# Kernel tuning notes

Measured on AMD Instinct MI355X. Metric: run time of the kernel, lower is better.

Reference implementation:

```python
import jax, jax.numpy as jnp
import numpy as np

B, T, D, DI, K, M, H, HD, L, VOCAB = 8, 512, 256, 512, 4, 2, 4, 64, 2, 272


def rmsnorm(x, w, eps=1e-6):
    return x * jax.lax.rsqrt(jnp.mean(x * x, axis=-1, keepdims=True) + eps) * w


def rotate_half(x):
    x1, x2 = x[..., ::2], x[..., 1::2]
    return jnp.stack([-x2, x1], axis=-1).reshape(x.shape)


def causal_conv(x, w, b):
    # x: [B,T,C], w: [C,K] depthwise causal conv, then silu
    y = jax.lax.conv_general_dilated(
        x.transpose(0, 2, 1), w[:, None, :],
        window_strides=(1,), padding=[(K - 1, 0)],
        feature_group_count=x.shape[-1])
    return jax.nn.silu(y.transpose(0, 2, 1) + b)


def delta_memory(x, Wv, Wg, Wb, Wa, A_log, dt_bias, Wblend, Wout):
    # x: [B,T,D]; per-timestep delta-rule fast-weight update with decay + key rotation
    Bv, Tn, Dm = x.shape
    vals = (x @ Wv).reshape(Bv, Tn, M, H, HD)
    gate = jax.nn.sigmoid(x @ Wg)                                   # [B,T,H]
    beta = jax.nn.sigmoid(jnp.einsum('btd,mdh->btmh', x, Wb))       # [B,T,M,H]
    alpha = jnp.einsum('btd,mdh->btmh', x, Wa) + dt_bias            # [B,T,M,H]
    decay = jnp.exp(-jnp.exp(A_log)[None, None] * jax.nn.softplus(alpha))
    blend = jax.nn.softmax((x @ Wblend).reshape(Bv, Tn, H, M), axis=-1)
    rk0 = x.reshape(Bv, Tn, H, HD)
    rk0 = rk0 / jnp.maximum(jnp.linalg.norm(rk0, axis=-1, keepdims=True), 1e-12)
    rks = [rk0]
    for _ in range(M - 1):
        rks.append(rotate_half(rks[-1]))
    rks = jnp.stack(rks, axis=2)                                    # [B,T,M,H,d]
    wks = jnp.pad(rks[:, :-1], ((0, 0), (1, 0), (0, 0), (0, 0), (0, 0)))  # shifted keys

    def step(S, inp):
        v, wk, rk, bt, dc, bl, g = inp
        S = S * dc[..., None, None]                                  # [B,M,H,d,d]
        pred = jnp.einsum('bmhdk,bmhd->bmhk', S, wk)
        err = (v - pred) * bt[..., None]
        S = S + wk[..., None] * err[..., None, :]                    # outer-product write
        read = jnp.einsum('bmhdk,bmhd->bmhk', S, rk)
        o = jnp.einsum('bhm,bmhk->bhk', bl, read) * g[..., None]
        return S, o

    tf = lambda a: jnp.moveaxis(a, 1, 0)
    xs = (tf(vals), tf(wks), tf(rks), tf(beta), tf(decay), tf(blend), tf(gate))
    S0 = jnp.zeros((Bv, M, H, HD, HD), x.dtype)
    _, o = jax.lax.scan(step, S0, xs)                                # [T,B,H,d]
    o = jnp.moveaxis(o, 0, 1).reshape(Bv, Tn, Dm)
    return x + o @ Wout


def setup_inputs():
    key = jax.random.key(0)
    ks = jax.random.split(key, 16)
    n = lambda k, shape, sc=0.02: jax.random.normal(k, shape, jnp.float32) * sc
    return {
        'ids': jax.random.randint(ks[0], (B, T), 0, VOCAB, jnp.int32),
        'emb': n(ks[1], (VOCAB, D)),
        'norm_w': jnp.ones((L, D), jnp.float32),
        'W_up': n(ks[2], (L, D, DI)),
        'W_gate': n(ks[3], (L, D, DI)),
        'W_down': n(ks[4], (L, DI, D)),
        'conv_w': n(ks[5], (L, DI, K), 0.1),
        'conv_b': jnp.zeros((L, DI), jnp.float32),
        'Wv': n(ks[6], (L, D, M * D)),
        'Wg': n(ks[7], (L, D, H)),
        'Wb': n(ks[8], (L, M, D, H)),
        'Wa': n(ks[9], (L, M, D, H)),
        'A_log': n(ks[10], (L, M, H), 0.5),
        'dt_bias': n(ks[11], (L, M, H), 0.5),
        'Wblend': n(ks[12], (L, D, H * M)),
        'Wout': n(ks[13], (L, D, D)),
        'final_norm_w': jnp.ones((D,), jnp.float32),
    }


def reference(ids, emb, norm_w, W_up, W_gate, W_down, conv_w, conv_b,
              Wv, Wg, Wb, Wa, A_log, dt_bias, Wblend, Wout, final_norm_w):
    x = emb[ids]
    for l in range(L):
        nx = rmsnorm(x, norm_w[l])
        h = causal_conv(nx @ W_up[l], conv_w[l], conv_b[l])
        out = (jax.nn.silu(nx @ W_gate[l]) * h) @ W_down[l]
        out = delta_memory(out, Wv[l], Wg[l], Wb[l], Wa[l],
                           A_log[l], dt_bias[l], Wblend[l], Wout[l])
        x = x + out
    return rmsnorm(x, final_norm_w) @ emb.T  # tied head
```

## Files before the change

### kernel.cpp

```cpp
#include <hip/hip_runtime.h>
#include <math.h>

#define BB 8
#define TT 512
#define DD 256
#define DIM 512
#define KW 4
#define MM 2
#define HH 4
#define HDIM 64
#define LL 2
#define VV 272

typedef __attribute__((ext_vector_type(8))) short bf16x8;
typedef __attribute__((ext_vector_type(4))) float f32x4;

__device__ __forceinline__ float sigf(float x){ return 1.f/(1.f+__expf(-x)); }
__device__ __forceinline__ float siluf(float x){ return x/(1.f+__expf(-x)); }

__device__ __forceinline__ unsigned short f2bf(float f){
  unsigned int u = __float_as_uint(f);
  unsigned int r = (u + 0x7FFFu + ((u >> 16) & 1u)) >> 16;
  return (unsigned short)r;
}
__device__ __forceinline__ float bf2f(unsigned short s){
  return __uint_as_float(((unsigned int)s) << 16);
}

__device__ __forceinline__ float xor1_add(float x){
  int y = __builtin_amdgcn_update_dpp(0, __float_as_int(x), 0xB1, 0xF, 0xF, true);
  return x + __int_as_float(y);
}
__device__ __forceinline__ float xor2_add(float x){
  int y = __builtin_amdgcn_update_dpp(0, __float_as_int(x), 0x4E, 0xF, 0xF, true);
  return x + __int_as_float(y);
}
__device__ __forceinline__ float ror4_add(float x){
  int y = __builtin_amdgcn_update_dpp(0, __float_as_int(x), 0x124, 0xF, 0xF, true);
  return x + __int_as_float(y);
}
__device__ __forceinline__ float ror8_add(float x){
  int y = __builtin_amdgcn_update_dpp(0, __float_as_int(x), 0x128, 0xF, 0xF, true);
  return x + __int_as_float(y);
}

__device__ __forceinline__ void gl_lds16(const void* g, void* l){
  __builtin_amdgcn_global_load_lds(
      (const __attribute__((address_space(1))) unsigned int*)g,
      (__attribute__((address_space(3))) unsigned int*)l,
      16, 0, 0);
}

#define LWB 589824
__global__ void k_cvt(const float* __restrict__ Wup, const float* __restrict__ Wgate,
                      const float* __restrict__ Wdown, const float* __restrict__ Wv,
                      const float* __restrict__ Wout, const float* __restrict__ emb,
                      const float* __restrict__ normw, const float* __restrict__ fnw,
                      unsigned short* __restrict__ wbf){
  int idx = blockIdx.x*256 + threadIdx.x;
  if (idx >= 2*LWB + VV*DD) return;
  float v;
  if (idx < 2*LWB){
    int l = (idx >= LWB) ? 1 : 0;
    int local = idx - l*LWB;
    if (local < 131072){ int n = local>>8, k = local&255;
      v = Wup[(size_t)l*131072 + k*DIM + n];
      if (l == 1) v *= normw[DD + k]; }
    else if (local < 262144){ local -= 131072; int n = local>>8, k = local&255;
      v = Wgate[(size_t)l*131072 + k*DIM + n];
      if (l == 1) v *= normw[DD + k]; }
    else if (local < 393216){ local -= 262144; int n = local>>9, k = local&511;
      v = Wdown[(size_t)l*131072 + k*DD + n]; }
    else if (local < 524288){ local -= 393216; int n = local>>8, k = local&255;
      v = Wv[(size_t)l*131072 + k*DIM + n]; }
    else { local -= 524288; int n = local>>8, k = local&255;
      v = Wout[(size_t)l*65536 + k*DD + n]; }
  } else {
    int k = (idx - 2*LWB) & 255;
    v = emb[idx - 2*LWB] * fnw[k];
  }
  wbf[idx] = f2bf(v);
}

__global__ void __launch_bounds__(256) k_embed_norm(const int* __restrict__ ids,
                                                    const float* __restrict__ emb,
                                                    const float* __restrict__ w,
                                                    float* __restrict__ x,
                                                    unsigned short* __restrict__ out){
  const int wv = threadIdx.x >> 6, l = threadIdx.x & 63;
  const int row = blockIdx.x*4 + wv;
  float4 v = *(const float4*)&emb[(size_t)ids[row]*DD + l*4];
  *(float4*)&x[(size_t)row*DD + l*4] = v;
  float ss = v.x*v.x + v.y*v.y + v.z*v.z + v.w*v.w;
  #pragma unroll
  for (int o = 32; o > 0; o >>= 1) ss += __shfl_xor(ss, o, 64);
  float sc = rsqrtf(ss*(1.f/DD) + 1e-6f);
  float4 wvv = *(const float4*)&w[l*4];
  ushort4 r;
  r.x = f2bf(v.x*sc*wvv.x); r.y = f2bf(v.y*sc*wvv.y);
  r.z = f2bf(v.z*sc*wvv.z); r.w = f2bf(v.w*sc*wvv.w);
  *(ushort4*)&out[(size_t)row*DD + l*4] = r;
}

template<int MODE>
__global__ void __launch_bounds__(256) k_gemm64(const unsigned short* __restrict__ A,
                                                const unsigned short* __restrict__ Bt,
                                                float* __restrict__ Cf,
                                                unsigned short* __restrict__ Cb,
                                                int N, int K){
  __shared__ unsigned short as[64][72];
  __shared__ unsigned short bs[64][72];
  const int tid = threadIdx.x;
  const int w = tid >> 6, l = tid & 63;
  const int m0 = blockIdx.y*64, n0 = blockIdx.x*64;
  const int ar = tid >> 2, ac = (tid & 3)*16;
  f32x4 acc[4] = {};
  for (int k0 = 0; k0 < K; k0 += 64){
    { const bf16x8* src = (const bf16x8*)&A[(size_t)(m0+ar)*K + k0 + ac];
      *(bf16x8*)&as[ar][ac]   = src[0];
      *(bf16x8*)&as[ar][ac+8] = src[1];
    }
    { int n = n0 + ar;
      bf16x8 z; z = (bf16x8)(short)0;
      bf16x8 b0 = z, b1 = z;
      if (n < N){
        const bf16x8* src = (const bf16x8*)&Bt[(size_t)n*K + k0 + ac];
        b0 = src[0]; b1 = src[1];
      }
      *(bf16x8*)&bs[ar][ac]   = b0;
      *(bf16x8*)&bs[ar][ac+8] = b1;
    }
    __syncthreads();
    const int mr = w*16 + (l & 15);
    const int kb = (l >> 4)*8;
    #pragma unroll
    for (int kc2 = 0; kc2 < 2; ++kc2){
      bf16x8 af = *(const bf16x8*)&as[mr][kc2*32 + kb];
      #pragma unroll
      for (int nt = 0; nt < 4; ++nt){
        bf16x8 bfr = *(const bf16x8*)&bs[nt*16 + (l & 15)][kc2*32 + kb];
        acc[nt] = __builtin_amdgcn_mfma_f32_16x16x32_bf16(af, bfr, acc[nt], 0, 0, 0);
      }
    }
    __syncthreads();
  }
  #pragma unroll
  for (int nt = 0; nt < 4; ++nt){
    int col = n0 + nt*16 + (l & 15);
    if (col < N){
      #pragma unroll
      for (int r = 0; r < 4; ++r){
        int row = m0 + w*16 + (l >> 4)*4 + r;
        if (MODE == 0 || MODE == 2) Cf[(size_t)row*N + col] = acc[nt][r];
        if (MODE == 1 || MODE == 2) Cb[(size_t)row*N + col] = f2bf(acc[nt][r]);
      }
    }
  }
}

__global__ void __launch_bounds__(256) k_gemmlogit(const float* __restrict__ X,
                                                   const float* __restrict__ pssq,
                                                   const unsigned short* __restrict__ Bt,
                                                   float* __restrict__ Cf,
                                                   int N, int K){
  __shared__ unsigned short as[64][72];
  __shared__ unsigned short bs[64][72];
  const int tid = threadIdx.x;
  const int w = tid >> 6, l = tid & 63;
  const int m0 = blockIdx.y*64, n0 = blockIdx.x*64;
  const int ar = tid >> 2, ac = (tid & 3)*16;
  const int arow = m0 + ar;
  const int ROWS = BB*TT;
  float ssq = pssq[arow] + pssq[ROWS + arow] + pssq[2*ROWS + arow] + pssq[3*ROWS + arow];
  const float sc = rsqrtf(ssq*(1.f/DD) + 1e-6f);
  f32x4 acc[4] = {};
  for (int k0 = 0; k0 < K; k0 += 64){
    { const float* src = &X[(size_t)arow*K + k0 + ac];
      #pragma unroll
      for (int j = 0; j < 4; ++j){
        float4 a = *(const float4*)&src[j*4];
        ushort4 u = make_ushort4(f2bf(a.x*sc), f2bf(a.y*sc), f2bf(a.z*sc), f2bf(a.w*sc));
        *(ushort4*)&as[ar][ac + j*4] = u;
      }
    }
    { int n = n0 + ar;
      bf16x8 z; z = (bf16x8)(short)0;
      bf16x8 b0 = z, b1 = z;
      if (n < N){
        const bf16x8* src = (const bf16x8*)&Bt[(size_t)n*K + k0 + ac];
        b0 = src[0]; b1 = src[1];
      }
      *(bf16x8*)&bs[ar][ac]   = b0;
      *(bf16x8*)&bs[ar][ac+8] = b1;
    }
    __syncthreads();
    const int mr = w*16 + (l & 15);
    const int kb = (l >> 4)*8;
    #pragma unroll
    for (int kc2 = 0; kc2 < 2; ++kc2){
      bf16x8 af = *(const bf16x8*)&as[mr][kc2*32 + kb];
      #pragma unroll
      for (int nt = 0; nt < 4; ++nt){
        bf16x8 bfr = *(const bf16x8*)&bs[nt*16 + (l & 15)][kc2*32 + kb];
        acc[nt] = __builtin_amdgcn_mfma_f32_16x16x32_bf16(af, bfr, acc[nt], 0, 0, 0);
      }
    }
    __syncthreads();
  }
  #pragma unroll
  for (int nt = 0; nt < 4; ++nt){
    int col = n0 + nt*16 + (l & 15);
    if (col < N){
      #pragma unroll
      for (int r = 0; r < 4; ++r){
        int row = m0 + w*16 + (l >> 4)*4 + r;
        Cf[(size_t)row*N + col] = acc[nt][r];
      }
    }
  }
}

template<int MODE>
__global__ void __launch_bounds__(256) k_gemm128(const unsigned short* __restrict__ A,
                                                 const unsigned short* __restrict__ Bt,
                                                 float* __restrict__ Cf,
                                                 unsigned short* __restrict__ Cb,
                                                 int N, int K){
  __shared__ unsigned short as[128][72];
  __shared__ unsigned short bs[64][72];
  const int tid = threadIdx.x;
  const int w = tid >> 6, l = tid & 63;
  const int m0 = blockIdx.y*128, n0 = blockIdx.x*64;
  const int ar = tid >> 1, ac = (tid & 1)*32;
  const int br = tid >> 2, bc = (tid & 3)*16;
  f32x4 acc[2][4] = {};
  for (int k0 = 0; k0 < K; k0 += 64){
    { const bf16x8* src = (const bf16x8*)&A[(size_t)(m0+ar)*K + k0 + ac];
      *(bf16x8*)&as[ar][ac]    = src[0];
      *(bf16x8*)&as[ar][ac+8]  = src[1];
      *(bf16x8*)&as[ar][ac+16] = src[2];
      *(bf16x8*)&as[ar][ac+24] = src[3];
    }
    { int n = n0 + br;
      bf16x8 z; z = (bf16x8)(short)0;
      bf16x8 b0 = z, b1 = z;
      if (n < N){
        const bf16x8* s = (const bf16x8*)&Bt[(size_t)n*K + k0 + bc];
        b0 = s[0]; b1 = s[1];
      }
      *(bf16x8*)&bs[br][bc]   = b0;
      *(bf16x8*)&bs[br][bc+8] = b1;
    }
    __syncthreads();
    const int lr = l & 15, kb = (l >> 4)*8;
    #pragma unroll
    for (int kc2 = 0; kc2 < 2; ++kc2){
      bf16x8 af0 = *(const bf16x8*)&as[w*32 + lr][kc2*32 + kb];
      bf16x8 af1 = *(const bf16x8*)&as[w*32 + 16 + lr][kc2*32 + kb];
      #pragma unroll
      for (int nt = 0; nt < 4; ++nt){
        bf16x8 bfr = *(const bf16x8*)&bs[nt*16 + lr][kc2*32 + kb];
        acc[0][nt] = __builtin_amdgcn_mfma_f32_16x16x32_bf16(af0, bfr, acc[0][nt], 0, 0, 0);
        acc[1][nt] = __builtin_amdgcn_mfma_f32_16x16x32_bf16(af1, bfr, acc[1][nt], 0, 0, 0);
      }
    }
    __syncthreads();
  }
  const int lr = l & 15;
  #pragma unroll
  for (int mt = 0; mt < 2; ++mt){
    #pragma unroll
    for (int nt = 0; nt < 4; ++nt){
      int col = n0 + nt*16 + lr;
      if (col < N){
        #pragma unroll
        for (int r = 0; r < 4; ++r){
          int row = m0 + w*32 + mt*16 + (l >> 4)*4 + r;
          if (MODE == 0 || MODE == 2) Cf[(size_t)row*N + col] = acc[mt][nt][r];
          if (MODE == 1 || MODE == 2) Cb[(size_t)row*N + col] = f2bf(acc[mt][nt][r]);
        }
      }
    }
  }
}

__global__ void __launch_bounds__(256) k_gemm_up(const unsigned short* __restrict__ A,
                                                 const unsigned short* __restrict__ But,
                                                 const unsigned short* __restrict__ Bgt,
                                                 unsigned short* __restrict__ Cu,
                                                 unsigned short* __restrict__ Cg){
  __shared__ unsigned short as[128][72];
  __shared__ unsigned short bu[64][72];
  __shared__ unsigned short bg[64][72];
  const int tid = threadIdx.x;
  const int w = tid >> 6, l = tid & 63;
  const int m0 = blockIdx.y*128, n0 = blockIdx.x*64;
  const int ar = tid >> 1, ac = (tid & 1)*32;
  const int br = tid >> 2, bc = (tid & 3)*16;
  f32x4 accu[2][4] = {}; f32x4 accg[2][4] = {};
  for (int k0 = 0; k0 < DD; k0 += 64){
    { const bf16x8* src = (const bf16x8*)&A[(size_t)(m0+ar)*DD + k0 + ac];
      *(bf16x8*)&as[ar][ac]    = src[0];
      *(bf16x8*)&as[ar][ac+8]  = src[1];
      *(bf16x8*)&as[ar][ac+16] = src[2];
      *(bf16x8*)&as[ar][ac+24] = src[3];
    }
    { const bf16x8* s0 = (const bf16x8*)&But[(size_t)(n0+br)*DD + k0 + bc];
      *(bf16x8*)&bu[br][bc]   = s0[0];
      *(bf16x8*)&bu[br][bc+8] = s0[1];
      const bf16x8* s1 = (const bf16x8*)&Bgt[(size_t)(n0+br)*DD + k0 + bc];
      *(bf16x8*)&bg[br][bc]   = s1[0];
      *(bf16x8*)&bg[br][bc+8] = s1[1];
    }
    __syncthreads();
    const int lr = l & 15, kb = (l >> 4)*8;
    #pragma unroll
    for (int kc2 = 0; kc2 < 2; ++kc2){
      bf16x8 af0 = *(const bf16x8*)&as[w*32 + lr][kc2*32 + kb];
      bf16x8 af1 = *(const bf16x8*)&as[w*32 + 16 + lr][kc2*32 + kb];
      #pragma unroll
      for (int nt = 0; nt < 4; ++nt){
        bf16x8 b0 = *(const bf16x8*)&bu[nt*16 + lr][kc2*32 + kb];
        accu[0][nt] = __builtin_amdgcn_mfma_f32_16x16x32_bf16(af0, b0, accu[0][nt], 0, 0, 0);
        accu[1][nt] = __builtin_amdgcn_mfma_f32_16x16x32_bf16(af1, b0, accu[1][nt], 0, 0, 0);
        bf16x8 b1 = *(const bf16x8*)&bg[nt*16 + lr][kc2*32 + kb];
        accg[0][nt] = __builtin_amdgcn_mfma_f32_16x16x32_bf16(af0, b1, accg[0][nt], 0, 0, 0);
        accg[1][nt] = __builtin_amdgcn_mfma_f32_16x16x32_bf16(af1, b1, accg[1][nt], 0, 0, 0);
      }
    }
    __syncthreads();
  }
  const int lr = l & 15;
  #pragma unroll
  for (int mt = 0; mt < 2; ++mt){
    #pragma unroll
    for (int nt = 0; nt < 4; ++nt){
      int col = n0 + nt*16 + lr;
      #pragma unroll
      for (int r = 0; r < 4; ++r){
        int row = m0 + w*32 + mt*16 + (l >> 4)*4 + r;
        Cu[(size_t)row*DIM + col] = f2bf(accu[mt][nt][r]);
        Cg[(size_t)row*DIM + col] = f2bf(accg[mt][nt][r]);
      }
    }
  }
}

__global__ void __launch_bounds__(256) k_gemm_up2(const float* __restrict__ X,
                                                  const float* __restrict__ pssq,
                                                  const unsigned short* __restrict__ But,
                                                  const unsigned short* __restrict__ Bgt,
                                                  unsigned short* __restrict__ Cu,
                                                  unsigned short* __restrict__ Cg){
  __shared__ unsigned short as[128][72];
  __shared__ unsigned short bu[64][72];
  __shared__ unsigned short bg[64][72];
  const int tid = threadIdx.x;
  const int w = tid >> 6, l = tid & 63;
  const int m0 = blockIdx.y*128, n0 = blockIdx.x*64;
  const int ar = tid >> 1, ac = (tid & 1)*32;
  const int br = tid >> 2, bc = (tid & 3)*16;
  const int arow = m0 + ar;
  const int ROWS = BB*TT;
  float ssq = pssq[arow] + pssq[ROWS + arow] + pssq[2*ROWS + arow] + pssq[3*ROWS + arow];
  const float sc = rsqrtf(ssq*(1.f/DD) + 1e-6f);
  f32x4 accu[2][4] = {}; f32x4 accg[2][4] = {};
  for (int k0 = 0; k0 < DD; k0 += 64){
    { const float* src = &X[(size_t)arow*DD + k0 + ac];
      #pragma unroll
      for (int j = 0; j < 8; ++j){
        float4 a = *(const float4*)&src[j*4];
        ushort4 u = make_ushort4(f2bf(a.x*sc), f2bf(a.y*sc), f2bf(a.z*sc), f2bf(a.w*sc));
        *(ushort4*)&as[ar][ac + j*4] = u;
      }
    }
    { const bf16x8* s0 = (const bf16x8*)&But[(size_t)(n0+br)*DD + k0 + bc];
      *(bf16x8*)&bu[br][bc]   = s0[0];
      *(bf16x8*)&bu[br][bc+8] = s0[1];
      const bf16x8* s1 = (const bf16x8*)&Bgt[(size_t)(n0+br)*DD + k0 + bc];
      *(bf16x8*)&bg[br][bc]   = s1[0];
      *(bf16x8*)&bg[br][bc+8] = s1[1];
    }
    __syncthreads();
    const int lr = l & 15, kb = (l >> 4)*8;
    #pragma unroll
    for (int kc2 = 0; kc2 < 2; ++kc2){
      bf16x8 af0 = *(const bf16x8*)&as[w*32 + lr][kc2*32 + kb];
      bf16x8 af1 = *(const bf16x8*)&as[w*32 + 16 + lr][kc2*32 + kb];
      #pragma unroll
      for (int nt = 0; nt < 4; ++nt){
        bf16x8 b0 = *(const bf16x8*)&bu[nt*16 + lr][kc2*32 + kb];
        accu[0][nt] = __builtin_amdgcn_mfma_f32_16x16x32_bf16(af0, b0, accu[0][nt], 0, 0, 0);
        accu[1][nt] = __builtin_amdgcn_mfma_f32_16x16x32_bf16(af1, b0, accu[1][nt], 0, 0, 0);
        bf16x8 b1 = *(const bf16x8*)&bg[nt*16 + lr][kc2*32 + kb];
        accg[0][nt] = __builtin_amdgcn_mfma_f32_16x16x32_bf16(af0, b1, accg[0][nt], 0, 0, 0);
        accg[1][nt] = __builtin_amdgcn_mfma_f32_16x16x32_bf16(af1, b1, accg[1][nt], 0, 0, 0);
      }
    }
    __syncthreads();
  }
  const int lr = l & 15;
  #pragma unroll
  for (int mt = 0; mt < 2; ++mt){
    #pragma unroll
    for (int nt = 0; nt < 4; ++nt){
      int col = n0 + nt*16 + lr;
      #pragma unroll
      for (int r = 0; r < 4; ++r){
        int row = m0 + w*32 + mt*16 + (l >> 4)*4 + r;
        Cu[(size_t)row*DIM + col] = f2bf(accu[mt][nt][r]);
        Cg[(size_t)row*DIM + col] = f2bf(accg[mt][nt][r]);
      }
    }
  }
}

__global__ void __launch_bounds__(256) k_gemm_wout(const float* __restrict__ p0,
                                                   const float* __restrict__ p1,
                                                   const unsigned short* __restrict__ Bt,
                                                   const float* __restrict__ y,
                                                   float* __restrict__ x,
                                                   float* __restrict__ rowssq){
  __shared__ unsigned short as[64][72];
  __shared__ unsigned short bs[64][72];
  const int tid = threadIdx.x;
  const int w = tid >> 6, l = tid & 63;
  const int m0 = blockIdx.y*64, n0 = blockIdx.x*64;
  const int ar = tid >> 2, ac = (tid & 3)*16;
  f32x4 acc[4] = {};
  for (int k0 = 0; k0 < DD; k0 += 64){
    #pragma unroll
    for (int j = 0; j < 4; ++j){
      size_t off = (size_t)(m0+ar)*DD + k0 + ac + j*4;
      float4 a = *(const float4*)&p0[off];
      float4 b = *(const float4*)&p1[off];
      a.x += b.x; a.y += b.y; a.z += b.z; a.w += b.w;
      ushort4 u = make_ushort4(f2bf(a.x), f2bf(a.y), f2bf(a.z), f2bf(a.w));
      *(ushort4*)&as[ar][ac + j*4] = u;
    }
    { const bf16x8* src = (const bf16x8*)&Bt[(size_t)(n0+ar)*DD + k0 + ac];
      *(bf16x8*)&bs[ar][ac]   = src[0];
      *(bf16x8*)&bs[ar][ac+8] = src[1];
    }
    __syncthreads();
    const int mr = w*16 + (l & 15);
    const int kb = (l >> 4)*8;
    #pragma unroll
    for (int kc2 = 0; kc2 < 2; ++kc2){
      bf16x8 af = *(const bf16x8*)&as[mr][kc2*32 + kb];
      #pragma unroll
      for (int nt = 0; nt < 4; ++nt){
        bf16x8 bfr = *(const bf16x8*)&bs[nt*16 + (l & 15)][kc2*32 + kb];
        acc[nt] = __builtin_amdgcn_mfma_f32_16x16x32_bf16(af, bfr, acc[nt], 0, 0, 0);
      }
    }
    __syncthreads();
  }
  const int ROWS = BB*TT;
  float ssq[4] = {0.f, 0.f, 0.f, 0.f};
  #pragma unroll
  for (int nt = 0; nt < 4; ++nt){
    int col = n0 + nt*16 + (l & 15);
    #pragma unroll
    for (int r = 0; r < 4; ++r){
      int row = m0 + w*16 + (l >> 4)*4 + r;
      size_t off = (size_t)row*DD + col;
      float nv = x[off] + y[off] + acc[nt][r];
      x[off] = nv;
      ssq[r] = fmaf(nv, nv, ssq[r]);
    }
  }
  #pragma unroll
  for (int r = 0; r < 4; ++r){
    float s = ssq[r];
    s = xor1_add(s); s = xor2_add(s); s = ror4_add(s); s = ror8_add(s);
    if ((l & 15) == 0){
      int row = m0 + w*16 + (l >> 4)*4 + r;
      rowssq[(size_t)blockIdx.x*ROWS + row] = s;
    }
  }
}

__global__ void k_conv(const unsigned short* __restrict__ u,
                       const unsigned short* __restrict__ g,
                       const float* __restrict__ cw, const float* __restrict__ cb,
                       unsigned short* __restrict__ hh){
  int i8 = blockIdx.x*256 + threadIdx.x;
  int cg = i8 & 63;
  int bt = i8 >> 6;
  int t  = bt & (TT-1);
  int c0 = cg*8;
  float acc[8];
  { float4 b0 = *(const float4*)&cb[c0];
    float4 b1 = *(const float4*)&cb[c0+4];
    acc[0]=b0.x; acc[1]=b0.y; acc[2]=b0.z; acc[3]=b0.w;
    acc[4]=b1.x; acc[5]=b1.y; acc[6]=b1.z; acc[7]=b1.w; }
  float wts[8][4];
  #pragma unroll
  for (int i = 0; i < 8; ++i) *(float4*)&wts[i][0] = *(const float4*)&cw[(c0+i)*KW];
  #pragma unroll
  for (int j = 0; j < KW; ++j){
    int dt_ = j - (KW-1);
    if (t + dt_ >= 0){
      bf16x8 uv = *(const bf16x8*)&u[(size_t)(bt + dt_)*DIM + c0];
      #pragma unroll
      for (int i = 0; i < 8; ++i)
        acc[i] = fmaf(bf2f((unsigned short)uv[i]), wts[i][j], acc[i]);
    }
  }
  bf16x8 gv = *(const bf16x8*)&g[(size_t)bt*DIM + c0];
  bf16x8 o;
  #pragma unroll
  for (int i = 0; i < 8; ++i){
    float h = siluf(acc[i]);
    o[i] = (short)f2bf(siluf(bf2f((unsigned short)gv[i])) * h);
  }
  *(bf16x8*)&hh[(size_t)bt*DIM + c0] = o;
}

__global__ void __launch_bounds__(256) k_fused(const float* __restrict__ y,
    const float* __restrict__ Wg, const float* __restrict__ Wb,
    const float* __restrict__ Wa, const float* __restrict__ Wbl,
    const float* __restrict__ A_log, const float* __restrict__ dtb,
    float* __restrict__ rkb, float* __restrict__ scal){
  __shared__ float s_y[4][260];
  __shared__ float s_p[4][32];
  const int wv = threadIdx.x >> 6, l = threadIdx.x & 63;
  const int row = blockIdx.x*4 + wv;

  float4 yv = *(const float4*)&y[(size_t)row*DD + l*4];
  *(float4*)&s_y[wv][l*4] = yv;

  float ss = yv.x*yv.x + yv.y*yv.y + yv.z*yv.z + yv.w*yv.w;
  ss = xor1_add(ss); ss = xor2_add(ss);
  ss = ror4_add(ss); ss = ror8_add(ss);
  float inv = 1.f / fmaxf(sqrtf(ss), 1e-12f);
  float4 rv; rv.x = yv.x*inv; rv.y = yv.y*inv; rv.z = yv.z*inv; rv.w = yv.w*inv;
  *(float4*)&rkb[(size_t)row*DD + l*4] = rv;

  __syncthreads();

  const int j = (l < 28) ? l : 27;
  const float* wp; int stride;
  if (j < 4){ wp = Wg + j; stride = HH; }
  else if (j < 12){ int m=(j-4)>>2, h=(j-4)&3; wp = Wb + (size_t)m*DD*HH + h; stride = HH; }
  else if (j < 20){ int m=(j-12)>>2, h=(j-12)&3; wp = Wa + (size_t)m*DD*HH + h; stride = HH; }
  else { wp = Wbl + (j-20); stride = HH*MM; }
  float a0=0.f,a1=0.f,a2=0.f,a3=0.f;
  #pragma unroll 4
  for (int k = 0; k < DD; k += 4){
    a0 = fmaf(s_y[wv][k+0], wp[(k+0)*stride], a0);
    a1 = fmaf(s_y[wv][k+1], wp[(k+1)*stride], a1);
    a2 = fmaf(s_y[wv][k+2], wp[(k+2)*stride], a2);
    a3 = fmaf(s_y[wv][k+3], wp[(k+3)*stride], a3);
  }
  if (l < 28) s_p[wv][l] = (a0+a1)+(a2+a3);

  __syncthreads();

  if (l < 8){
    int m = l >> 2, h = l & 3;
    float gs  = sigf(s_p[wv][h]);
    float btv = sigf(s_p[wv][4 + m*4 + h]);
    float sp  = s_p[wv][12 + m*4 + h] + dtb[m*HH + h];
    sp = (sp > 15.f) ? sp : log1pf(__expf(sp));
    float dc  = __expf(-__expf(A_log[m*HH + h]) * sp);
    float l0 = s_p[wv][20 + h*2], l1 = s_p[wv][20 + h*2 + 1];
    float mx = fmaxf(l0, l1);
    float e0 = __expf(l0-mx), e1 = __expf(l1-mx);
    float bl = (m ? e1 : e0) / (e0 + e1);
    float4 o; o.x = dc; o.y = btv; o.z = bl*gs; o.w = 0.f;
    *(float4*)&scal[((size_t)row*MM + m)*(HH*4) + h*4] = o;
  }
}

#define SSTEP(T_, WK, RK, PF, VB, SB) { \
  const float dc = SB.x, btv = SB.y, blg = SB.z; \
  const float v = VB; \
  { const int tn_ = ((T_)+2 < 64) ? (T_)+2 : 63; \
    PF = *(const float4*)&s_rk[p][tn_][dbase]; \
    VB = bf2f(s_v[p][tn_][vidx]); \
    SB = *(const float4*)&s_sc[p][tn_][0]; } \
  const float err = (v - dc*rrc)*btv; \
  float rr0=0.f, rr1=0.f; \
  { const float4 rp = WK; const float4 rc = RK; \
    float w0,w1,w2,w3,c0,c1,c2,c3; \
    if (ROT == 0){ w0=rp.x; w1=rp.y; w2=rp.z; w3=rp.w; c0=rc.x; c1=rc.y; c2=rc.z; c3=rc.w; } \
    else { w0=-rp.y; w1=rp.x; w2=-rp.w; w3=rp.z; c0=-rc.y; c1=rc.x; c2=-rc.w; c3=rc.z; } \
    S[0] = fmaf(S[0], dc, w0*err); rr0 = fmaf(S[0], c0, rr0); \
    S[1] = fmaf(S[1], dc, w1*err); rr1 = fmaf(S[1], c1, rr1); \
    S[2] = fmaf(S[2], dc, w2*err); rr0 = fmaf(S[2], c2, rr0); \
    S[3] = fmaf(S[3], dc, w3*err); rr1 = fmaf(S[3], c3, rr1); } \
  float rr = rr0 + rr1; \
  rr = xor1_add(rr); rr = xor2_add(rr); rr = ror4_add(rr); rr = ror8_add(rr); \
  rrc = rr; \
  if (seg == 0) part[(size_t)(rowchunk + (T_))*DD + h*HDIM + kq4*4 + klocal] = blg*rr; \
}

template<int ROT>
__device__ __forceinline__ void scan_body(int b, int h, int kq4, int l,
    const unsigned short* __restrict__ vals, const float* __restrict__ rkb,
    const float* __restrict__ scal, float* __restrict__ part,
    float (*s_rk)[64][64], unsigned short (*s_v)[64][8], float (*s_sc)[64][4])
{
  const int seg = l & 15, klocal = l >> 4;
  const int dbase = seg*4;
  const int vidx = (kq4 & 1)*4 + klocal;
  const int kq8 = kq4 >> 1;
  const int rowbase = b*TT;

  float S[4];
  #pragma unroll
  for (int j = 0; j < 4; ++j) S[j] = 0.f;
  const float4 Z = make_float4(0.f,0.f,0.f,0.f);
  float4 rb0 = Z, rb1 = Z, rb2 = Z, rb3 = Z;
  float vb0 = 0.f, vb1 = 0.f;
  float4 sb0 = Z, sb1 = Z;
  float rrc = 0.f;

  auto stage = [&](int c, int pbuf){
    const int r0 = rowbase + c*64;
    #pragma unroll
    for (int i = 0; i < 16; ++i){
      const float* g = rkb + (size_t)(r0 + i*4 + (l>>4))*DD + h*HDIM + (l&15)*4;
      gl_lds16(g, &s_rk[pbuf][i*4][0]);
    }
    { const unsigned short* g = vals + ((size_t)(r0 + l)*MM + ROT)*DD + h*HDIM + kq8*8;
      gl_lds16(g, &s_v[pbuf][0][0]); }
    { const float* g = scal + ((size_t)(r0 + l)*MM + ROT)*(HH*4) + h*4;
      gl_lds16(g, &s_sc[pbuf][0][0]); }
  };

  stage(0, 0);
  for (int c = 0; c < TT/64; ++c){
    const int p = c & 1;
    __syncthreads();
    if (c + 1 < TT/64) stage(c+1, p^1);
    rb0 = *(const float4*)&s_rk[p][0][dbase];
    rb1 = *(const float4*)&s_rk[p][1][dbase];
    vb0 = bf2f(s_v[p][0][vidx]); vb1 = bf2f(s_v[p][1][vidx]);
    sb0 = *(const float4*)&s_sc[p][0][0]; sb1 = *(const float4*)&s_sc[p][1][0];
    const int rowchunk = rowbase + c*64;
    for (int tt = 0; tt < 64; tt += 4){
      SSTEP(tt+0, rb3, rb0, rb2, vb0, sb0)
      SSTEP(tt+1, rb0, rb1, rb3, vb1, sb1)
      SSTEP(tt+2, rb1, rb2, rb0, vb0, sb0)
      SSTEP(tt+3, rb2, rb3, rb1, vb1, sb1)
    }
  }
}

__global__ void __launch_bounds__(64) k_scan(const unsigned short* __restrict__ vals,
                                             const float* __restrict__ rkb,
                                             const float* __restrict__ scal,
                                             float* __restrict__ partials){
  __shared__ float s_rk[2][64][64];
  __shared__ unsigned short s_v[2][64][8];
  __shared__ float s_sc[2][64][4];
  const int bi = blockIdx.x;
  const int kq4 = bi & 15;
  const int m  = (bi >> 4) & 1;
  const int h  = (bi >> 5) & 3;
  const int b  = bi >> 7;
  float* part = partials + (size_t)m*(BB*TT*DD);
  if (m == 0) scan_body<0>(b, h, kq4, threadIdx.x, vals, rkb, scal, part, s_rk, s_v, s_sc);
  else        scan_body<1>(b, h, kq4, threadIdx.x, vals, rkb, scal, part, s_rk, s_v, s_sc);
}

extern "C" void kernel_launch(void* const* d_in, const int* in_sizes, int n_in,
                              void* d_out, int out_size, void* d_ws, size_t ws_size,
                              hipStream_t stream){
  const int*   ids   = (const int*)d_in[0];
  const float* emb   = (const float*)d_in[1];
  const float* normw = (const float*)d_in[2];
  const float* Wup   = (const float*)d_in[3];
  const float* Wgate = (const float*)d_in[4];
  const float* Wdown = (const float*)d_in[5];
  const float* convw = (const float*)d_in[6];
  const float* convb = (const float*)d_in[7];
  const float* Wv    = (const float*)d_in[8];
  const float* Wg    = (const float*)d_in[9];
  const float* Wb    = (const float*)d_in[10];
  const float* Wa    = (const float*)d_in[11];
  const float* A_log = (const float*)d_in[12];
  const float* dtb   = (const float*)d_in[13];
  const float* Wbl   = (const float*)d_in[14];
  const float* Wout  = (const float*)d_in[15];
  const float* fnw   = (const float*)d_in[16];
  float* out = (float*)d_out;

  const int ROWS = BB*TT;
  const size_t MEG = 1u << 20;
  float* ws   = (float*)d_ws;
  float* x    = ws;
  unsigned short* nyb = (unsigned short*)(x + MEG);
  float* big1 = x + MEG + MEG/2;
  float* big2 = big1 + 2*MEG;
  float* y    = big2 + 2*MEG;
  float* rkb  = y    + MEG;
  float* scal = rkb  + MEG;
  float* rowssq = scal + (1u<<17);
  unsigned short* wbf = (unsigned short*)(rowssq + 4*ROWS);

  unsigned short* ub  = (unsigned short*)big1;
  unsigned short* gb  = (unsigned short*)(big1 + MEG);
  unsigned short* valsb = ub;

  { int total = 2*LWB + VV*DD;
    k_cvt<<<(total + 255)/256, 256, 0, stream>>>(Wup, Wgate, Wdown, Wv, Wout, emb,
                                                 normw, fnw, wbf); }

  k_embed_norm<<<ROWS/4, 256, 0, stream>>>(ids, emb, normw, x, nyb);

  for (int l = 0; l < LL; ++l){
    unsigned short* wl = wbf + (size_t)l*LWB;
    unsigned short* upT   = wl;
    unsigned short* gateT = wl + 131072;
    unsigned short* downT = wl + 262144;
    unsigned short* wvT   = wl + 393216;
    unsigned short* woutT = wl + 524288;

    if (l == 0)
      k_gemm_up<<<dim3(DIM/64, ROWS/128), 256, 0, stream>>>(nyb, upT, gateT, ub, gb);
    else
      k_gemm_up2<<<dim3(DIM/64, ROWS/128), 256, 0, stream>>>(x, rowssq, upT, gateT, ub, gb);
    k_conv<<<(ROWS*DIM/8)/256, 256, 0, stream>>>(ub, gb, convw + l*DIM*KW, convb + l*DIM, gb);
    k_gemm64<2><<<dim3(DD/64, ROWS/64), 256, 0, stream>>>(gb, downT, y, nyb, DD, DIM);
    k_gemm128<1><<<dim3(DIM/64, ROWS/128), 256, 0, stream>>>(nyb, wvT, nullptr, valsb, DIM, DD);
    k_fused<<<ROWS/4, 256, 0, stream>>>(y, Wg + l*DD*HH, Wb + (size_t)l*MM*DD*HH,
                                        Wa + (size_t)l*MM*DD*HH, Wbl + l*DD*HH*MM,
                                        A_log + l*MM*HH, dtb + l*MM*HH, rkb, scal);
    k_scan<<<BB*HH*MM*16, 64, 0, stream>>>(valsb, rkb, scal, big2);
    k_gemm_wout<<<dim3(DD/64, ROWS/64), 256, 0, stream>>>(big2, big2 + MEG, woutT, y, x, rowssq);
  }

  unsigned short* embT = wbf + 2*LWB;
  k_gemmlogit<<<dim3((VV+63)/64, ROWS/64), 256, 0, stream>>>(x, rowssq, embT, out, VV, DD);
}
```

Measured before the change: 284.9 us.

## Fuse causal depthwise conv and SiLU gating into the up/gate GEMM epilogue

Merges the separate conv kernel into the up/gate projection GEMM. The up-projection tile is staged in shared memory with a 3-row halo, and the halo rows are recomputed by scalar dot products per block. The epilogue then applies the causal conv, bias, SiLU and gate directly and writes only the final hidden activation. This removes one launch and the round trip of writing and re-reading the full up and gate tensors, at the cost of redundant halo compute, extra shared memory and one more barrier.

```diff
diff --git a/kernel.cpp b/kernel.cpp
--- a/kernel.cpp
+++ b/kernel.cpp
@@ -284,26 +284,89 @@
   }
 }
 
-__global__ void __launch_bounds__(256) k_gemm_up(const unsigned short* __restrict__ A,
-                                                 const unsigned short* __restrict__ But,
-                                                 const unsigned short* __restrict__ Bgt,
-                                                 unsigned short* __restrict__ Cu,
-                                                 unsigned short* __restrict__ Cg){
+template<int L>
+__global__ void __launch_bounds__(256) k_gemm_upc(
+    const unsigned short* __restrict__ Anyb,
+    const float* __restrict__ X, const float* __restrict__ pssq,
+    const unsigned short* __restrict__ But,
+    const unsigned short* __restrict__ Bgt,
+    const float* __restrict__ cw, const float* __restrict__ cb,
+    unsigned short* __restrict__ Chh)
+{
   __shared__ unsigned short as[128][72];
   __shared__ unsigned short bu[64][72];
   __shared__ unsigned short bg[64][72];
+  __shared__ unsigned short s_ub[132][68];
+  __shared__ float s_cw[64][4];
+  __shared__ float s_cb[64];
   const int tid = threadIdx.x;
   const int w = tid >> 6, l = tid & 63;
   const int m0 = blockIdx.y*128, n0 = blockIdx.x*64;
   const int ar = tid >> 1, ac = (tid & 1)*32;
   const int br = tid >> 2, bc = (tid & 3)*16;
+  const int ROWS = BB*TT;
+  const int t0 = m0 & (TT-1);
+
+  float scA = 1.f;
+  if (L == 1){
+    const int arow = m0 + ar;
+    float ssq = pssq[arow] + pssq[ROWS + arow] + pssq[2*ROWS + arow] + pssq[3*ROWS + arow];
+    scA = rsqrtf(ssq*(1.f/DD) + 1e-6f);
+  }
+
+  if (tid < 192){
+    int i = tid >> 6;
+    int c = tid & 63;
+    float acc = 0.f;
+    if (t0 != 0){
+      int grow = m0 - 3 + i;
+      const unsigned short* bptr = &But[(size_t)(n0+c)*DD];
+      if (L == 0){
+        const unsigned short* a = &Anyb[(size_t)grow*DD];
+        for (int k = 0; k < DD; k += 8){
+          bf16x8 av = *(const bf16x8*)&a[k];
+          bf16x8 bv = *(const bf16x8*)&bptr[k];
+          #pragma unroll
+          for (int e = 0; e < 8; ++e)
+            acc = fmaf(bf2f((unsigned short)av[e]), bf2f((unsigned short)bv[e]), acc);
+        }
+      } else {
+        float ssq = pssq[grow] + pssq[ROWS + grow] + pssq[2*ROWS + grow] + pssq[3*ROWS + grow];
+        float sc = rsqrtf(ssq*(1.f/DD) + 1e-6f);
+        const float* a = &X[(size_t)grow*DD];
+        for (int k = 0; k < DD; k += 4){
+          float4 av = *(const float4*)&a[k];
+          #pragma unroll
+          for (int e = 0; e < 4; ++e){
+            float ae = bf2f(f2bf(((const float*)&av)[e]*sc));
+            acc = fmaf(ae, bf2f(bptr[k+e]), acc);
+          }
+        }
+      }
+    }
+    s_ub[tid >> 6][tid & 63] = (t0 != 0) ? f2bf(acc) : (unsigned short)0;
+  }
+  if (tid < 64){
+    *(float4*)&s_cw[tid][0] = *(const float4*)&cw[(n0+tid)*KW];
+    s_cb[tid] = cb[n0+tid];
+  }
+
   f32x4 accu[2][4] = {}; f32x4 accg[2][4] = {};
   for (int k0 = 0; k0 < DD; k0 += 64){
-    { const bf16x8* src = (const bf16x8*)&A[(size_t)(m0+ar)*DD + k0 + ac];
+    if (L == 0){
+      const bf16x8* src = (const bf16x8*)&Anyb[(size_t)(m0+ar)*DD + k0 + ac];
       *(bf16x8*)&as[ar][ac]    = src[0];
       *(bf16x8*)&as[ar][ac+8]  = src[1];
       *(bf16x8*)&as[ar][ac+16] = src[2];
       *(bf16x8*)&as[ar][ac+24] = src[3];
+    } else {
+      const float* src = &X[(size_t)(m0+ar)*DD + k0 + ac];
+      #pragma unroll
+      for (int j = 0; j < 8; ++j){
+        float4 a = *(const float4*)&src[j*4];
+        ushort4 u = make_ushort4(f2bf(a.x*scA), f2bf(a.y*scA), f2bf(a.z*scA), f2bf(a.w*scA));
+        *(ushort4*)&as[ar][ac + j*4] = u;
+      }
     }
     { const bf16x8* s0 = (const bf16x8*)&But[(size_t)(n0+br)*DD + k0 + bc];
       *(bf16x8*)&bu[br][bc]   = s0[0];
@@ -330,89 +393,35 @@
     }
     __syncthreads();
   }
+
   const int lr = l & 15;
   #pragma unroll
-  for (int mt = 0; mt < 2; ++mt){
-    #pragma unroll
-    for (int nt = 0; nt < 4; ++nt){
-      int col = n0 + nt*16 + lr;
+  for (int mt = 0; mt < 2; ++mt)
+    #pragma unroll
+    for (int nt = 0; nt < 4; ++nt)
       #pragma unroll
       for (int r = 0; r < 4; ++r){
-        int row = m0 + w*32 + mt*16 + (l >> 4)*4 + r;
-        Cu[(size_t)row*DIM + col] = f2bf(accu[mt][nt][r]);
-        Cg[(size_t)row*DIM + col] = f2bf(accg[mt][nt][r]);
-      }
-    }
-  }
-}
-
-__global__ void __launch_bounds__(256) k_gemm_up2(const float* __restrict__ X,
-                                                  const float* __restrict__ pssq,
-                                                  const unsigned short* __restrict__ But,
-                                                  const unsigned short* __restrict__ Bgt,
-                                                  unsigned short* __restrict__ Cu,
-                                                  unsigned short* __restrict__ Cg){
-  __shared__ unsigned short as[128][72];
-  __shared__ unsigned short bu[64][72];
-  __shared__ unsigned short bg[64][72];
-  const int tid = threadIdx.x;
-  const int w = tid >> 6, l = tid & 63;
-  const int m0 = blockIdx.y*128, n0 = blockIdx.x*64;
-  const int ar = tid >> 1, ac = (tid & 1)*32;
-  const int br = tid >> 2, bc = (tid & 3)*16;
-  const int arow = m0 + ar;
-  const int ROWS = BB*TT;
-  float ssq = pssq[arow] + pssq[ROWS + arow] + pssq[2*ROWS + arow] + pssq[3*ROWS + arow];
-  const float sc = rsqrtf(ssq*(1.f/DD) + 1e-6f);
-  f32x4 accu[2][4] = {}; f32x4 accg[2][4] = {};
-  for (int k0 = 0; k0 < DD; k0 += 64){
-    { const float* src = &X[(size_t)arow*DD + k0 + ac];
-      #pragma unroll
-      for (int j = 0; j < 8; ++j){
-        float4 a = *(const float4*)&src[j*4];
-        ushort4 u = make_ushort4(f2bf(a.x*sc), f2bf(a.y*sc), f2bf(a.z*sc), f2bf(a.w*sc));
-        *(ushort4*)&as[ar][ac + j*4] = u;
-      }
-    }
-    { const bf16x8* s0 = (const bf16x8*)&But[(size_t)(n0+br)*DD + k0 + bc];
-      *(bf16x8*)&bu[br][bc]   = s0[0];
-      *(bf16x8*)&bu[br][bc+8] = s0[1];
-      const bf16x8* s1 = (const bf16x8*)&Bgt[(size_t)(n0+br)*DD + k0 + bc];
-      *(bf16x8*)&bg[br][bc]   = s1[0];
-      *(bf16x8*)&bg[br][bc+8] = s1[1];
-    }
-    __syncthreads();
-    const int lr = l & 15, kb = (l >> 4)*8;
-    #pragma unroll
-    for (int kc2 = 0; kc2 < 2; ++kc2){
-      bf16x8 af0 = *(const bf16x8*)&as[w*32 + lr][kc2*32 + kb];
-      bf16x8 af1 = *(const bf16x8*)&as[w*32 + 16 + lr][kc2*32 + kb];
-      #pragma unroll
-      for (int nt = 0; nt < 4; ++nt){
-        bf16x8 b0 = *(const bf16x8*)&bu[nt*16 + lr][kc2*32 + kb];
-        accu[0][nt] = __builtin_amdgcn_mfma_f32_16x16x32_bf16(af0, b0, accu[0][nt], 0, 0, 0);
-        accu[1][nt] = __builtin_amdgcn_mfma_f32_16x16x32_bf16(af1, b0, accu[1][nt], 0, 0, 0);
-        bf16x8 b1 = *(const bf16x8*)&bg[nt*16 + lr][kc2*32 + kb];
-        accg[0][nt] = __builtin_amdgcn_mfma_f32_16x16x32_bf16(af0, b1, accg[0][nt], 0, 0, 0);
-        accg[1][nt] = __builtin_amdgcn_mfma_f32_16x16x32_bf16(af1, b1, accg[1][nt], 0, 0, 0);
-      }
-    }
-    __syncthreads();
-  }
-  const int lr = l & 15;
-  #pragma unroll
-  for (int mt = 0; mt < 2; ++mt){
-    #pragma unroll
-    for (int nt = 0; nt < 4; ++nt){
-      int col = n0 + nt*16 + lr;
+        int trow = w*32 + mt*16 + (l >> 4)*4 + r;
+        s_ub[3 + trow][nt*16 + lr] = f2bf(accu[mt][nt][r]);
+      }
+  __syncthreads();
+
+  #pragma unroll
+  for (int mt = 0; mt < 2; ++mt)
+    #pragma unroll
+    for (int nt = 0; nt < 4; ++nt)
       #pragma unroll
       for (int r = 0; r < 4; ++r){
-        int row = m0 + w*32 + mt*16 + (l >> 4)*4 + r;
-        Cu[(size_t)row*DIM + col] = f2bf(accu[mt][nt][r]);
-        Cg[(size_t)row*DIM + col] = f2bf(accg[mt][nt][r]);
-      }
-    }
-  }
+        int trow = w*32 + mt*16 + (l >> 4)*4 + r;
+        int cl = nt*16 + lr;
+        float a0 = s_cb[cl];
+        #pragma unroll
+        for (int j = 0; j < KW; ++j)
+          a0 = fmaf(bf2f(s_ub[trow + j][cl]), s_cw[cl][j], a0);
+        float h = siluf(a0);
+        float o = siluf(accg[mt][nt][r]) * h;
+        Chh[(size_t)(m0 + trow)*DIM + (n0 + cl)] = f2bf(o);
+      }
 }
 
 __global__ void __launch_bounds__(256) k_gemm_wout(const float* __restrict__ p0,
@@ -479,43 +488,6 @@
       rowssq[(size_t)blockIdx.x*ROWS + row] = s;
     }
   }
-}
-
-__global__ void k_conv(const unsigned short* __restrict__ u,
-                       const unsigned short* __restrict__ g,
-                       const float* __restrict__ cw, const float* __restrict__ cb,
-                       unsigned short* __restrict__ hh){
-  int i8 = blockIdx.x*256 + threadIdx.x;
-  int cg = i8 & 63;
-  int bt = i8 >> 6;
-  int t  = bt & (TT-1);
-  int c0 = cg*8;
-  float acc[8];
-  { float4 b0 = *(const float4*)&cb[c0];
-    float4 b1 = *(const float4*)&cb[c0+4];
-    acc[0]=b0.x; acc[1]=b0.y; acc[2]=b0.z; acc[3]=b0.w;
-    acc[4]=b1.x; acc[5]=b1.y; acc[6]=b1.z; acc[7]=b1.w; }
-  float wts[8][4];
-  #pragma unroll
-  for (int i = 0; i < 8; ++i) *(float4*)&wts[i][0] = *(const float4*)&cw[(c0+i)*KW];
-  #pragma unroll
-  for (int j = 0; j < KW; ++j){
-    int dt_ = j - (KW-1);
-    if (t + dt_ >= 0){
-      bf16x8 uv = *(const bf16x8*)&u[(size_t)(bt + dt_)*DIM + c0];
-      #pragma unroll
-      for (int i = 0; i < 8; ++i)
-        acc[i] = fmaf(bf2f((unsigned short)uv[i]), wts[i][j], acc[i]);
-    }
-  }
-  bf16x8 gv = *(const bf16x8*)&g[(size_t)bt*DIM + c0];
-  bf16x8 o;
-  #pragma unroll
-  for (int i = 0; i < 8; ++i){
-    float h = siluf(acc[i]);
-    o[i] = (short)f2bf(siluf(bf2f((unsigned short)gv[i])) * h);
-  }
-  *(bf16x8*)&hh[(size_t)bt*DIM + c0] = o;
 }
 
 __global__ void __launch_bounds__(256) k_fused(const float* __restrict__ y,
@@ -702,9 +674,8 @@
   float* rowssq = scal + (1u<<17);
   unsigned short* wbf = (unsigned short*)(rowssq + 4*ROWS);
 
-  unsigned short* ub  = (unsigned short*)big1;
   unsigned short* gb  = (unsigned short*)(big1 + MEG);
-  unsigned short* valsb = ub;
+  unsigned short* valsb = (unsigned short*)big1;
 
   { int total = 2*LWB + VV*DD;
     k_cvt<<<(total + 255)/256, 256, 0, stream>>>(Wup, Wgate, Wdown, Wv, Wout, emb,
@@ -721,10 +692,11 @@
     unsigned short* woutT = wl + 524288;
 
     if (l == 0)
-      k_gemm_up<<<dim3(DIM/64, ROWS/128), 256, 0, stream>>>(nyb, upT, gateT, ub, gb);
+      k_gemm_upc<0><<<dim3(DIM/64, ROWS/128), 256, 0, stream>>>(
+          nyb, nullptr, nullptr, upT, gateT, convw + l*DIM*KW, convb + l*DIM, gb);
     else
-      k_gemm_up2<<<dim3(DIM/64, ROWS/128), 256, 0, stream>>>(x, rowssq, upT, gateT, ub, gb);
-    k_conv<<<(ROWS*DIM/8)/256, 256, 0, stream>>>(ub, gb, convw + l*DIM*KW, convb + l*DIM, gb);
+      k_gemm_upc<1><<<dim3(DIM/64, ROWS/128), 256, 0, stream>>>(
+          nullptr, x, rowssq, upT, gateT, convw + l*DIM*KW, convb + l*DIM, gb);
     k_gemm64<2><<<dim3(DD/64, ROWS/64), 256, 0, stream>>>(gb, downT, y, nyb, DD, DIM);
     k_gemm128<1><<<dim3(DIM/64, ROWS/128), 256, 0, stream>>>(nyb, wvT, nullptr, valsb, DIM, DD);
     k_fused<<<ROWS/4, 256, 0, stream>>>(y, Wg + l*DD*HH, Wb + (size_t)l*MM*DD*HH,
```

Result: faster. 274.5 us (-3.7%).
